# Performance work log

Measured on AMD Instinct MI355X. Metric: run time of the kernel, lower is better.

Reference implementation:

```python
import jax, jax.numpy as jnp
import numpy as np

TAU = 3.0          # CPG tau
VTH = 1.0          # LIF v_threshold (v_reset = 0, hard reset)
PEAK = 16          # peak population size
NUM_E = 25         # int(32 * 0.8) excitatory neurons
FATIGUE_TH = 8
ALPHA = 4.0        # spikingjelly sigmoid surrogate alpha (unused in fwd)


def spike_fn(x):
    # Heaviside threshold at 0 (v >= VTH fires)
    return (x >= 0.0).astype(x.dtype)


def setup_inputs() -> dict:
    key = jax.random.key(0)
    k0, k1, k2, k3, k4 = jax.random.split(key, 5)
    B, N = 524288, 32
    spike_history = (jax.random.uniform(k0, (B, N)) < 0.3).astype(jnp.float32)
    neighbor_E_spikes = (jax.random.uniform(k1, (B, 8, NUM_E)) < 0.3).astype(jnp.float32)
    # mutual_inhibition: -2.0 everywhere, within-population blocks *0.1 -> -0.2,
    # cross-population blocks set to -3.0
    is_peak = jnp.arange(N) < PEAK
    same_pop = is_peak[:, None] == is_peak[None, :]
    mutual_inhibition = jnp.where(same_pop, -0.2, -3.0).astype(jnp.float32)
    coupling_W = jax.random.normal(k2, (N, NUM_E), dtype=jnp.float32) * 0.2
    peak_fatigue = jax.random.randint(k3, (B,), 0, 10, dtype=jnp.int32)
    trough_fatigue = jax.random.randint(k4, (B,), 0, 10, dtype=jnp.int32)
    v0 = jnp.zeros((B, N), dtype=jnp.float32)
    return {
        "spike_history": spike_history,
        "neighbor_E_spikes": neighbor_E_spikes,
        "mutual_inhibition": mutual_inhibition,
        "coupling_W": coupling_W,
        "v0": v0,
        "peak_fatigue": peak_fatigue,
        "trough_fatigue": trough_fatigue,
        "num_ticks": 5,
    }


def reference(spike_history, neighbor_E_spikes, mutual_inhibition, coupling_W,
              v0, peak_fatigue, trough_fatigue, num_ticks):
    B = spike_history.shape[0]
    # fatigue-driven drive: trough fatigue excites peak half, peak fatigue excites trough half
    dp = jnp.where(trough_fatigue >= FATIGUE_TH, 2.0, 0.0)[:, None]  # [B,1]
    dt = jnp.where(peak_fatigue >= FATIGUE_TH, 2.0, 0.0)[:, None]
    drive = jnp.concatenate(
        [jnp.broadcast_to(dp, (B, PEAK)), jnp.broadcast_to(dt, (B, 32 - PEAK))], axis=-1)
    # neighbor coupling: sum_k W @ nbr_k ; constant across ticks, hoisted out of loop
    coupling = jnp.einsum('bkn,mn->bm', neighbor_E_spikes, coupling_W)
    base = drive + 0.3 * coupling  # [B,32]

    def step(carry, _):
        v, sh, acc = carry
        recurrent = jnp.einsum('bn,mn->bm', sh, mutual_inhibition)  # sh @ M.T
        x = base + 0.5 * recurrent
        # LIF (decay_input=True): v += (x - (v - v_reset)) / tau, v_reset = 0
        v = v + (x - v) / TAU
        s = spike_fn(v - VTH)
        v = v * (1.0 - s)  # hard reset to 0
        return (v, s, acc + s), None

    init = (v0, spike_history, jnp.zeros_like(v0))
    (v, sh, acc), _ = jax.lax.scan(step, init, None, length=num_ticks)
    should_stay = acc[:, PEAK:].sum(axis=-1) > 0.5  # trough active => STAY
    return acc[:, :NUM_E], should_stay
```

## Files before the change

kernel.cpp:

```cpp
#include <hip/hip_runtime.h>


#define FATIGUE_TH 8

__global__ __launch_bounds__(256) void AgentLSM_70841190580507_kernel(
    const float* __restrict__ sh_in,
    const float* __restrict__ nbr,
    const float* __restrict__ M,
    const float* __restrict__ W,
    const int*   __restrict__ pf,
    const int*   __restrict__ tf,
    const int*   __restrict__ ticks_p,
    float* __restrict__ out_acc,
    float* __restrict__ out_stay,
    int B, int nchunks)
{
    __shared__ float4 lds_nbr4[400];
    __shared__ float  lds_cnt[8 * 28];
    __shared__ float  lds_out[200];
    __shared__ float  lds_stay[8];

    float* lds_nbr = (float*)lds_nbr4;

    const int tid = threadIdx.x;
    const int g   = tid >> 5;
    const int m   = tid & 31;
    const bool is_peak = (m < 16);

    float w[28];
    #pragma unroll
    for (int n = 0; n < 25; ++n) w[n] = W[m * 25 + n];
    w[25] = 0.f; w[26] = 0.f; w[27] = 0.f;

    const float a_same  = M[0];
    const float a_cross = M[16];
    const int T = ticks_p[0];

    for (int chunk = blockIdx.x; chunk < nchunks; chunk += gridDim.x) {
        const long long b = (long long)chunk * 8 + g;
        const int nv = min(8, B - chunk * 8);
        const bool valid = (g < nv);

        const float4* nb4 = (const float4*)nbr + (long long)chunk * 400;
        if (nv == 8) {
            #pragma unroll
            for (int i = tid; i < 400; i += 256) lds_nbr4[i] = nb4[i];
        } else {
            const long long ftot  = (long long)B * 200;
            const long long fbase = (long long)chunk * 1600;
            for (int i = tid; i < 400; i += 256) {
                long long f0 = fbase + (long long)i * 4;
                lds_nbr4[i] = (f0 + 3 < ftot) ? nb4[i]
                                              : make_float4(0.f, 0.f, 0.f, 0.f);
            }
        }

        float drive = 0.f;
        int init_bit = 0;
        if (valid) {
            drive = is_peak ? ((tf[b] >= FATIGUE_TH) ? 2.0f : 0.0f)
                            : ((pf[b] >= FATIGUE_TH) ? 2.0f : 0.0f);
            init_bit = (sh_in[b * 32 + m] != 0.0f);
        }

        __syncthreads();

        if (m < 28) {
            float c = 0.f;
            if (m < 25) {
                #pragma unroll
                for (int k = 0; k < 8; ++k) c += lds_nbr[g * 200 + k * 25 + m];
            }
            lds_cnt[g * 28 + m] = c;
        }

        __syncthreads();

        float coup = 0.f;
        {
            const float4* c4p = (const float4*)&lds_cnt[g * 28];
            #pragma unroll
            for (int q = 0; q < 7; ++q) {
                float4 c4 = c4p[q];
                coup += c4.x * w[4*q+0] + c4.y * w[4*q+1]
                      + c4.z * w[4*q+2] + c4.w * w[4*q+3];
            }
        }

        const float base = drive + 0.3f * coup;
        float v = 0.0f;

        unsigned long long bal = __ballot(init_bit);
        unsigned int mask = (unsigned int)(bal >> (tid & 32));

        int acc = 0;
        unsigned int any_tr = 0;

        #define TICK()  do {                                                   \
            float Spf = (float)__popc(mask & 0xFFFFu);                         \
            float Stf = (float)__popc(mask >> 16);                             \
            float rec = is_peak ? (a_same * Spf + a_cross * Stf)               \
                                : (a_cross * Spf + a_same * Stf);              \
            float x = base + 0.5f * rec;                                       \
            v = v + (x - v) / 3.0f;                  \
            bool s = (v >= 1.0f);                 \
            unsigned long long sb = __ballot(s);                               \
            mask = (unsigned int)(sb >> (tid & 32));                           \
            any_tr |= (mask >> 16);                                            \
            acc += s ? 1 : 0;                                                  \
            v = s ? 0.0f : v;                                                  \
        } while (0)

        if (T == 5) {
            TICK(); TICK(); TICK(); TICK(); TICK();
        } else {
            for (int t = 0; t < T; ++t) TICK();
        }
        #undef TICK

        if (m < 25) lds_out[g * 25 + m] = (float)acc;
        if (m == 31) lds_stay[g] = any_tr ? 1.0f : 0.0f;
        __syncthreads();

        const long long obase = (long long)chunk * 200;
        if (nv == 8) {
            if (tid < 50)
                ((float4*)out_acc)[obase / 4 + tid] =
                    ((const float4*)lds_out)[tid];
            if (tid < 8)
                out_stay[(long long)chunk * 8 + tid] = lds_stay[tid];
        } else {
            if (tid < nv * 25) out_acc[obase + tid] = lds_out[tid];
            if (tid < nv)      out_stay[(long long)chunk * 8 + tid] = lds_stay[tid];
        }
    }
}

extern "C" void kernel_launch(void* const* d_in, const int* in_sizes, int n_in,
                              void* d_out, int out_size, void* d_ws, size_t ws_size,
                              hipStream_t stream) {
    const float* sh    = (const float*)d_in[0];
    const float* nbr   = (const float*)d_in[1];
    const float* M     = (const float*)d_in[2];
    const float* W     = (const float*)d_in[3];
    const int*   pf    = (const int*)d_in[5];
    const int*   tf    = (const int*)d_in[6];
    const int*   ticks = (const int*)d_in[7];

    const int B = in_sizes[5];
    float* out_acc  = (float*)d_out;
    float* out_stay = out_acc + (long long)B * 25;

    const int nchunks = (B + 7) / 8;
    int blocks = nchunks < 2048 ? nchunks : 2048;
    AgentLSM_70841190580507_kernel<<<blocks, 256, 0, stream>>>(
        sh, nbr, M, W, pf, tf, ticks, out_acc, out_stay, B, nchunks);
}
```

Before: 680.7 us.

## Double-buffer neighbor spikes via async global-to-LDS loads with contiguous chunk ranges

Result: faster. 636.9 us (-6.4%).

```diff
diff --git a/kernel.cpp b/kernel.cpp
--- a/kernel.cpp
+++ b/kernel.cpp
@@ -3,7 +3,13 @@
 
 #define FATIGUE_TH 8
 
-__global__ __launch_bounds__(256) void AgentLSM_70841190580507_kernel(
+__device__ __forceinline__ void async_f4(const float* g, float* l) {
+    __builtin_amdgcn_global_load_lds(
+        (const __attribute__((address_space(1))) void*)g,
+        (__attribute__((address_space(3))) void*)l, 16, 0, 0);
+}
+
+__global__ __launch_bounds__(256, 4) void AgentLSM_70841190580507_kernel(
     const float* __restrict__ sh_in,
     const float* __restrict__ nbr,
     const float* __restrict__ M,
@@ -13,47 +19,57 @@
     const int*   __restrict__ ticks_p,
     float* __restrict__ out_acc,
     float* __restrict__ out_stay,
-    int B, int nchunks)
+    int B, int nchunks, int cpb)
 {
-    __shared__ float4 lds_nbr4[400];
-    __shared__ float  lds_cnt[8 * 28];
-    __shared__ float  lds_out[200];
-    __shared__ float  lds_stay[8];
-
-    float* lds_nbr = (float*)lds_nbr4;
+    __shared__ float lds_nbr[2][1600];
+    __shared__ float lds_cnt[8 * 28];
 
     const int tid = threadIdx.x;
     const int g   = tid >> 5;
     const int m   = tid & 31;
     const bool is_peak = (m < 16);
 
+    if (tid < 200) async_f4(W + tid * 4, &lds_nbr[0][tid * 4]);
+    __syncthreads();
     float w[28];
     #pragma unroll
-    for (int n = 0; n < 25; ++n) w[n] = W[m * 25 + n];
+    for (int n = 0; n < 25; ++n) w[n] = lds_nbr[0][m * 25 + n];
     w[25] = 0.f; w[26] = 0.f; w[27] = 0.f;
-
     const float a_same  = M[0];
     const float a_cross = M[16];
     const int T = ticks_p[0];
+    __syncthreads();
 
-    for (int chunk = blockIdx.x; chunk < nchunks; chunk += gridDim.x) {
-        const long long b = (long long)chunk * 8 + g;
-        const int nv = min(8, B - chunk * 8);
-        const bool valid = (g < nv);
+    const int first = blockIdx.x * cpb;
+    if (first >= nchunks) return;
+    const int count = min(cpb, nchunks - first);
 
-        const float4* nb4 = (const float4*)nbr + (long long)chunk * 400;
-        if (nv == 8) {
-            #pragma unroll
-            for (int i = tid; i < 400; i += 256) lds_nbr4[i] = nb4[i];
-        } else {
-            const long long ftot  = (long long)B * 200;
-            const long long fbase = (long long)chunk * 1600;
-            for (int i = tid; i < 400; i += 256) {
-                long long f0 = fbase + (long long)i * 4;
-                lds_nbr4[i] = (f0 + 3 < ftot) ? nb4[i]
-                                              : make_float4(0.f, 0.f, 0.f, 0.f);
-            }
-        }
+    #define STAGE(c, buf) do {                                                \
+        const float* _src = nbr + (long long)(c) * 1600;                      \
+        float* _dst = lds_nbr[(buf)];                                         \
+        if ((long long)((c) + 1) * 8 <= (long long)B) {                       \
+            async_f4(_src + tid * 4, _dst + tid * 4);                         \
+            if (tid < 144) async_f4(_src + (tid + 256) * 4,                   \
+                                    _dst + (tid + 256) * 4);                  \
+        } else {                 \
+            const long long _ftot = (long long)B * 200 - (long long)(c) * 1600;\
+            for (int _i = tid; _i < 400; _i += 256) {                         \
+                float4 _v = make_float4(0.f, 0.f, 0.f, 0.f);                  \
+                if ((long long)_i * 4 + 3 < _ftot)                            \
+                    _v = ((const float4*)_src)[_i];                           \
+                ((float4*)_dst)[_i] = _v;                                     \
+            }                                                                 \
+        }                                                                     \
+    } while (0)
+
+    STAGE(first, 0);
+    __syncthreads();
+
+    int cur = 0;
+    for (int j = 0; j < count; ++j) {
+        const int c = first + j;
+        const long long b = (long long)c * 8 + g;
+        const bool valid = (b < (long long)B);
 
         float drive = 0.f;
         int init_bit = 0;
@@ -63,18 +79,17 @@
             init_bit = (sh_in[b * 32 + m] != 0.0f);
         }
 
+        if (m < 28) {
+            float cv = 0.f;
+            if (m < 25) {
+                #pragma unroll
+                for (int k = 0; k < 8; ++k) cv += lds_nbr[cur][g * 200 + k * 25 + m];
+            }
+            lds_cnt[g * 28 + m] = cv;
+        }
         __syncthreads();
 
-        if (m < 28) {
-            float c = 0.f;
-            if (m < 25) {
-                #pragma unroll
-                for (int k = 0; k < 8; ++k) c += lds_nbr[g * 200 + k * 25 + m];
-            }
-            lds_cnt[g * 28 + m] = c;
-        }
-
-        __syncthreads();
+        if (j + 1 < count) STAGE(c + 1, cur ^ 1);
 
         float coup = 0.f;
         {
@@ -118,22 +133,15 @@
         }
         #undef TICK
 
-        if (m < 25) lds_out[g * 25 + m] = (float)acc;
-        if (m == 31) lds_stay[g] = any_tr ? 1.0f : 0.0f;
+        if (valid) {
+            if (m < 25) out_acc[(long long)c * 200 + g * 25 + m] = (float)acc;
+            if (m == 0) out_stay[b] = any_tr ? 1.0f : 0.0f;
+        }
+
         __syncthreads();
-
-        const long long obase = (long long)chunk * 200;
-        if (nv == 8) {
-            if (tid < 50)
-                ((float4*)out_acc)[obase / 4 + tid] =
-                    ((const float4*)lds_out)[tid];
-            if (tid < 8)
-                out_stay[(long long)chunk * 8 + tid] = lds_stay[tid];
-        } else {
-            if (tid < nv * 25) out_acc[obase + tid] = lds_out[tid];
-            if (tid < nv)      out_stay[(long long)chunk * 8 + tid] = lds_stay[tid];
-        }
+        cur ^= 1;
     }
+    #undef STAGE
 }
 
 extern "C" void kernel_launch(void* const* d_in, const int* in_sizes, int n_in,
@@ -152,7 +160,9 @@
     float* out_stay = out_acc + (long long)B * 25;
 
     const int nchunks = (B + 7) / 8;
-    int blocks = nchunks < 2048 ? nchunks : 2048;
-    AgentLSM_70841190580507_kernel<<<blocks, 256, 0, stream>>>(
-        sh, nbr, M, W, pf, tf, ticks, out_acc, out_stay, B, nchunks);
+    int grid = nchunks < 8192 ? nchunks : 8192;
+    int cpb  = (nchunks + grid - 1) / grid;
+    grid = (nchunks + cpb - 1) / cpb;
+    AgentLSM_70841190580507_kernel<<<grid, 256, 0, stream>>>(
+        sh, nbr, M, W, pf, tf, ticks, out_acc, out_stay, B, nchunks, cpb);
 }
```
